# Performance work log

Measured on AMD Instinct MI355X. Metric: run time of the kernel, lower is better.

## Reference

```python
import jax, jax.numpy as jnp
import numpy as np

B, T, N = 32, 512, 16
C, V, D, H, L = 150, 832, 512, 512, 5  # chord vocab, note vocab, embed dim, hidden, layers


def setup_inputs() -> dict:
    key = jax.random.key(0)
    ks = jax.random.split(key, 16)
    s = 0.05
    note = jax.random.randint(ks[0], (B, T, N), 0, V)
    chord = jax.random.randint(ks[1], (B, T), 0, C)
    chord_table = jax.random.normal(ks[2], (C, D), jnp.float32) * s
    note_table = jax.random.normal(ks[3], (V, D), jnp.float32) * s
    # GRU layer 0 (input = 2*D), layers 1..L-1 (input = H), gate order r,z,n like torch
    w_ih0 = jax.random.normal(ks[4], (3 * H, 2 * D), jnp.float32) * s
    w_hh0 = jax.random.normal(ks[5], (3 * H, H), jnp.float32) * s
    b_ih0 = jax.random.normal(ks[6], (3 * H,), jnp.float32) * s
    b_hh0 = jax.random.normal(ks[7], (3 * H,), jnp.float32) * s
    w_ih_r = jax.random.normal(ks[8], (L - 1, 3 * H, H), jnp.float32) * s
    w_hh_r = jax.random.normal(ks[9], (L - 1, 3 * H, H), jnp.float32) * s
    b_ih_r = jax.random.normal(ks[10], (L - 1, 3 * H), jnp.float32) * s
    b_hh_r = jax.random.normal(ks[11], (L - 1, 3 * H), jnp.float32) * s
    fc_w = jax.random.normal(ks[12], (C, H), jnp.float32) * s
    fc_b = jax.random.normal(ks[13], (C,), jnp.float32) * s
    return dict(note=note, chord=chord, chord_table=chord_table, note_table=note_table,
                w_ih0=w_ih0, w_hh0=w_hh0, b_ih0=b_ih0, b_hh0=b_hh0,
                w_ih_r=w_ih_r, w_hh_r=w_hh_r, b_ih_r=b_ih_r, b_hh_r=b_hh_r,
                fc_w=fc_w, fc_b=fc_b)


def _gru_layer(x, wih, whh, bih, bhh):
    # x: [B, T, in] -> [B, T, H], torch GRU cell math (gate order r,z,n)
    xp = jnp.einsum('bti,gi->btg', x, wih) + bih          # precompute input proj [B,T,3H]
    xp = jnp.swapaxes(xp, 0, 1)                            # [T,B,3H]
    h0 = jnp.zeros((x.shape[0], whh.shape[1]), x.dtype)

    def step(h, xpt):
        gh = h @ whh.T + bhh
        xr, xz, xn = jnp.split(xpt, 3, axis=-1)
        hr, hz, hn = jnp.split(gh, 3, axis=-1)
        r = jax.nn.sigmoid(xr + hr)
        z = jax.nn.sigmoid(xz + hz)
        n = jnp.tanh(xn + r * hn)
        h_new = (1.0 - z) * n + z * h
        return h_new, h_new

    _, ys = jax.lax.scan(step, h0, xp)
    return jnp.swapaxes(ys, 0, 1)                          # [B,T,H]


def _forward(note, chord, chord_table, note_table, w_ih0, w_hh0, b_ih0, b_hh0,
             w_ih_r, w_hh_r, b_ih_r, b_hh_r, fc_w, fc_b):
    # padding_idx=0: zero row 0 of both tables (also blocks its gradient)
    ct = chord_table.at[0].set(0.0)
    nt = note_table.at[0].set(0.0)
    chord_emb = ct[chord]                                   # [B,T,D]
    # ragged mean over notes before first zero; mask[k]=1 iff no zero in note[...,:k+1]
    mask = jnp.cumprod((note != 0).astype(chord_table.dtype), axis=-1)  # [B,T,N]
    emb = nt[note]                                          # [B,T,N,D]
    cnt = jnp.maximum(mask.sum(-1), 1.0)                    # zero_index==0 case -> mean of zero row
    note_emb = jnp.einsum('btnd,btn->btd', emb, mask) / cnt[..., None]
    x = jnp.concatenate([chord_emb, note_emb], axis=-1)     # [B,T,2D]
    x = _gru_layer(x, w_ih0, w_hh0, b_ih0, b_hh0)
    for l in range(w_ih_r.shape[0]):
        x = _gru_layer(x, w_ih_r[l], w_hh_r[l], b_ih_r[l], b_hh_r[l])
    return x @ fc_w.T + fc_b                                # [B,T,C]


def reference(note, chord, chord_table, note_table, w_ih0, w_hh0, b_ih0, b_hh0,
              w_ih_r, w_hh_r, b_ih_r, b_hh_r, fc_w, fc_b):
    return _forward(note, chord, chord_table, note_table, w_ih0, w_hh0, b_ih0, b_hh0,
                    w_ih_r, w_hh_r, b_ih_r, b_hh_r, fc_w, fc_b)
```

## Files before the change

kernel.cpp:

```cpp
#include <hip/hip_runtime.h>
#include <hip/hip_bf16.h>

#define B_   32
#define T_   512
#define NN_  16
#define CV_  150
#define D_   512
#define H_   512
#define BT_  16384
#define K0_  1024
#define G3H_ 1536
#define NBF_ 160
#define GXB_ 6144
#define WSZ_ 49152
#define XSLOT_ 16384
#define XRING_ 32
#define HRING_ 8
#define SENT32 0x7f7f7f7fu
#define HCAP 16384
#define XCAP 16384
#define BCAP 65536

using bf16x8 = __attribute__((ext_vector_type(8))) short;
using f32x4  = __attribute__((ext_vector_type(4))) float;
using u32x4  = __attribute__((ext_vector_type(4))) unsigned int;
typedef unsigned long long u64;

__device__ __forceinline__ unsigned short f2bf(float f){
  unsigned int u = __builtin_bit_cast(unsigned int, f);
  u += 0x7fffu + ((u >> 16) & 1u);
  return (unsigned short)(u >> 16);
}

__device__ __forceinline__ void store8(unsigned short* p, f32x4 a, f32x4 b){
  union { unsigned short us[8]; u32x4 v; } u;
  u.us[0]=f2bf(a[0]); u.us[1]=f2bf(a[1]); u.us[2]=f2bf(a[2]); u.us[3]=f2bf(a[3]);
  u.us[4]=f2bf(b[0]); u.us[5]=f2bf(b[1]); u.us[6]=f2bf(b[2]); u.us[7]=f2bf(b[3]);
  *(u32x4*)p = u.v;
}

__device__ __forceinline__ u64 ld_coh_u64(const u64* p){
  return __hip_atomic_load(p, __ATOMIC_RELAXED, __HIP_MEMORY_SCOPE_AGENT);
}
__device__ __forceinline__ void st_coh_u32(void* p, unsigned int v){
  __hip_atomic_store((unsigned int*)p, v, __ATOMIC_RELAXED, __HIP_MEMORY_SCOPE_AGENT);
}
__device__ __forceinline__ float ld_coh_f32(const float* p){
  return __hip_atomic_load(p, __ATOMIC_RELAXED, __HIP_MEMORY_SCOPE_AGENT);
}
__device__ __forceinline__ void st_coh_f32(float* p, float v){
  __hip_atomic_store((unsigned int*)p, __builtin_bit_cast(unsigned int, v),
                     __ATOMIC_RELAXED, __HIP_MEMORY_SCOPE_AGENT);
}
__device__ __forceinline__ void st_flag(int* p, int v){
  __hip_atomic_store(p, v, __ATOMIC_RELAXED, __HIP_MEMORY_SCOPE_AGENT);
}
__device__ __forceinline__ int ld_flag(const int* p){
  return __hip_atomic_load(p, __ATOMIC_RELAXED, __HIP_MEMORY_SCOPE_AGENT);
}

__device__ __forceinline__ bool bad64(u64 q){
  return ((unsigned int)q == SENT32) | ((unsigned int)(q >> 32) == SENT32);
}

__global__ void convert_bf16(const float* __restrict__ src,
                             unsigned short* __restrict__ dst, int n){
  int i = blockIdx.x * 256 + threadIdx.x;
  if (i < n) dst[i] = f2bf(src[i]);
}

__global__ void prep_wfrag(const float* __restrict__ whh0,
                           const float* __restrict__ whhr,
                           const float* __restrict__ wihr,
                           unsigned short* __restrict__ wsw, int total){
  int idx = blockIdx.x * 256 + threadIdx.x;
  if (idx >= total) return;
  int pos = idx & 511;
  int lam = pos >> 3, e = pos & 7;
  int fr  = idx >> 9;
  int ks  = fr & 31;
  int g   = (fr >> 5) % 3;
  int blk = fr / 96;
  int sub = blk & 31, l = blk >> 5;
  int row = g * 512 + sub * 16 + (lam & 15);
  int k   = (ks & 15) * 32 + (lam >> 4) * 8 + e;
  float v;
  if (l == 0) v = (ks < 16) ? whh0[(size_t)row * H_ + k] : 0.f;
  else {
    const float* w = (ks < 16) ? (whhr + (size_t)(l - 1) * G3H_ * H_)
                               : (wihr + (size_t)(l - 1) * G3H_ * H_);
    v = w[(size_t)row * H_ + k];
  }
  wsw[idx] = f2bf(v);
}

__global__ void prep_bias(const float* __restrict__ bhh0,
                          const float* __restrict__ bihr,
                          const float* __restrict__ bhhr,
                          float* __restrict__ bias_sw, int total){
  int idx = blockIdx.x * 256 + threadIdx.x;
  if (idx >= total) return;
  int q = idx & 3, u = (idx >> 2) & 15, sub = (idx >> 6) & 31, l = idx >> 11;
  int j = sub * 16 + u;
  float v;
  if (l == 0){
    v = (q == 0) ? bhh0[j] : (q == 1) ? bhh0[512 + j] : (q == 2) ? 0.f : bhh0[1024 + j];
  } else {
    const float* bi = bihr + (size_t)(l - 1) * G3H_;
    const float* bh = bhhr + (size_t)(l - 1) * G3H_;
    v = (q == 0) ? bi[j] + bh[j]
      : (q == 1) ? bi[512 + j] + bh[512 + j]
      : (q == 2) ? bi[1024 + j] : bh[1024 + j];
  }
  bias_sw[idx] = v;
}

__global__ __launch_bounds__(64) void emb_kernel(
    const int* __restrict__ note, const int* __restrict__ chord,
    const float* __restrict__ ctab, const float* __restrict__ ntab,
    unsigned short* __restrict__ x0){
  const int bt = blockIdx.x;
  const int tid = threadIdx.x;
  __shared__ int sn[NN_];
  if (tid < NN_) sn[tid] = note[bt * NN_ + tid];
  __syncthreads();
  float alive = 1.f, cnt = 0.f;
  float msk[NN_];
  #pragma unroll
  for (int k = 0; k < NN_; ++k){ if (sn[k] == 0) alive = 0.f; msk[k] = alive; cnt += alive; }
  const float inv = 1.f / fmaxf(cnt, 1.f);
  const int ch = chord[bt];
  const int d0 = tid * 8;
  f32x4 c0 = {0.f,0.f,0.f,0.f}, c1 = {0.f,0.f,0.f,0.f};
  if (ch != 0){
    const float* cp = ctab + (size_t)ch * D_ + d0;
    c0 = *(const f32x4*)cp; c1 = *(const f32x4*)(cp + 4);
  }
  f32x4 s0 = {0.f,0.f,0.f,0.f}, s1 = {0.f,0.f,0.f,0.f};
  #pragma unroll
  for (int k = 0; k < NN_; ++k){
    if (msk[k] != 0.f){
      const float* np = ntab + (size_t)sn[k] * D_ + d0;
      s0 += *(const f32x4*)np;
      s1 += *(const f32x4*)(np + 4);
    }
  }
  s0 *= inv; s1 *= inv;
  unsigned short* o = x0 + (size_t)bt * K0_ + d0;
  store8(o, c0, c1);
  store8(o + D_, s0, s1);
}

__global__ __launch_bounds__(256) void gemm_bt(
    const unsigned short* __restrict__ X, const unsigned short* __restrict__ W,
    const float* __restrict__ bias, float* __restrict__ Y,
    int M, int N, int K, int wmode){
  const int lane = threadIdx.x & 63;
  const int wave = threadIdx.x >> 6;
  const int l15 = lane & 15, kq4 = lane >> 4;
  const int m_frag = blockIdx.y * 64 + wave * 16 + l15;
  const int n_base = blockIdx.x * 64;
  f32x4 acc[4] = {{0.f,0.f,0.f,0.f},{0.f,0.f,0.f,0.f},{0.f,0.f,0.f,0.f},{0.f,0.f,0.f,0.f}};
  const unsigned short* xptr = X + (size_t)m_frag * K + kq4 * 8;
  const unsigned short* wptr[4];
  #pragma unroll
  for (int i = 0; i < 4; ++i){
    int n = n_base + i * 16 + l15;
    if (n >= N) n = N - 1;
    wptr[i] = W + (size_t)n * K + kq4 * 8;
  }
  for (int k0 = 0; k0 < K; k0 += 32){
    bf16x8 a = *(const bf16x8*)(xptr + k0);
    #pragma unroll
    for (int i = 0; i < 4; ++i){
      bf16x8 b = *(const bf16x8*)(wptr[i] + k0);
      acc[i] = __builtin_amdgcn_mfma_f32_16x16x32_bf16(a, b, acc[i], 0, 0, 0);
    }
  }
  const int mrow = blockIdx.y * 64 + wave * 16 + kq4 * 4;
  #pragma unroll
  for (int i = 0; i < 4; ++i){
    int n = n_base + i * 16 + l15;
    if (n < N){
      float bv = bias[n];
      #pragma unroll
      for (int r = 0; r < 4; ++r){
        int m = mrow + r;
        float v = acc[i][r] + bv;
        if (wmode == 0) Y[(size_t)m * N + n] = v;
        else            Y[((size_t)(m & (T_-1)) * N + n) * B_ + (m >> 9)] = v;
      }
    }
  }
}

union Ufrag { u64 q[2]; bf16x8 v; };

__global__ __launch_bounds__(256, 1) void gru_fused(
    float* xp, const unsigned short* __restrict__ wsw,
    const float* __restrict__ bias_sw, unsigned short* hT,
    unsigned short* xT, unsigned short* xout, int* cprog,
    const unsigned short* __restrict__ x0g,
    const unsigned short* __restrict__ wih0g,
    const float* __restrict__ bih0g, int* gprog){
  __shared__ unsigned short w_s[96 * 512];
  __shared__ float p_s[2][4][2][2][16][16];

  const int tid = threadIdx.x;
  const int blk = blockIdx.x;

  if (blk >= NBF_){
    const int idx = blk - NBF_;
    const int gx  = idx % 24;
    const int gyy = idx / 24;
    const int bb  = gyy & 31, tc = gyy >> 5;
    const int m0  = bb * 512 + tc * 64;
    const int lane = tid & 63, wave = tid >> 6;
    const int l15 = lane & 15, kq4 = lane >> 4;
    const int m_frag = m0 + wave * 16 + l15;
    const int n_base = gx * 64;
    f32x4 acc[4] = {{0.f,0.f,0.f,0.f},{0.f,0.f,0.f,0.f},{0.f,0.f,0.f,0.f},{0.f,0.f,0.f,0.f}};
    const unsigned short* xptr = x0g + (size_t)m_frag * K0_ + kq4 * 8;
    const unsigned short* wptr[4];
    #pragma unroll
    for (int i = 0; i < 4; ++i){
      int n = n_base + i * 16 + l15;
      wptr[i] = wih0g + (size_t)n * K0_ + kq4 * 8;
    }
    for (int k0 = 0; k0 < K0_; k0 += 32){
      bf16x8 a = *(const bf16x8*)(xptr + k0);
      #pragma unroll
      for (int i = 0; i < 4; ++i){
        bf16x8 b = *(const bf16x8*)(wptr[i] + k0);
        acc[i] = __builtin_amdgcn_mfma_f32_16x16x32_bf16(a, b, acc[i], 0, 0, 0);
      }
    }
    const int mrow = m0 + wave * 16 + kq4 * 4;
    #pragma unroll
    for (int i = 0; i < 4; ++i){
      int n = n_base + i * 16 + l15;
      float bv = bih0g[n];
      #pragma unroll
      for (int r = 0; r < 4; ++r){
        int m = mrow + r;
        float v = acc[i][r] + bv;
        st_coh_f32(&xp[((size_t)(m & (T_-1)) * G3H_ + n) * B_ + (m >> 9)], v);
      }
    }
    asm volatile("s_waitcnt vmcnt(0)" ::: "memory");
    __syncthreads();
    if (tid == 0) atomicAdd(&gprog[tc], 1);
    return;
  }

  const int l   = blk >> 5;
  const int sub = blk & 31;

  {
    const u32x4* src = (const u32x4*)(wsw + (size_t)blk * WSZ_);
    u32x4* dst = (u32x4*)w_s;
    #pragma unroll
    for (int i = 0; i < 24; ++i) dst[tid + 256 * i] = src[tid + 256 * i];
  }
  __syncthreads();

  const int lane = tid & 63, wave = tid >> 6;
  const int l15 = lane & 15, l4 = lane >> 4;
  const int myn = wave >> 1;
  const int kh  = wave & 1;
  const int myb = (myn << 4) + l15;
  const int fro = (l4 << 3);
  const int khofs = kh * 256;
  const int khb = kh * 8;

  const int cb = tid & 31;
  const int cj = (tid >> 5) * 2;
  const int jg = sub * 16 + cj;
  const float* bsp = bias_sw + blk * 64;
  const float br0 = bsp[cj*4+0],     bz0 = bsp[cj*4+1],     bx0 = bsp[cj*4+2],     bn0 = bsp[cj*4+3];
  const float br1 = bsp[(cj+1)*4+0], bz1 = bsp[(cj+1)*4+1], bx1 = bsp[(cj+1)*4+2], bn1 = bsp[(cj+1)*4+3];
  float hres0 = 0.f, hres1 = 0.f;

  unsigned short* hTl = hT + (size_t)l * (HRING_ * 32 * 512);
  unsigned short* xTw = xT + (size_t)(l < 4 ? l : 0) * ((size_t)XRING_ * XSLOT_);
  const unsigned short* xTr = xT + (size_t)(l > 0 ? l - 1 : 0) * ((size_t)XRING_ * XSLOT_);
  const int* bp_own = cprog + (l << 5);
  int*       bp_pub = cprog + ((l > 0 ? l - 1 : 0) << 5);

  float era=0,eza=0,ena=0,era1=0,eza1=0,ena1=0;
  float erb=0,ezb=0,enb=0,erb1=0,ezb1=0,enb1=0;
  if (l == 0){
    if (tid == 0){
      int itc = 0;
      while (ld_flag(&gprog[0]) < 768){
        if (++itc > (1 << 24)) break;
        __builtin_amdgcn_s_sleep(8);
      }
    }
    __syncthreads();
    { const float* xq = xp + (size_t)0 * (G3H_ * B_) + cb;
      era=ld_coh_f32(&xq[(size_t)(0*H_+jg)*B_]); era1=ld_coh_f32(&xq[(size_t)(0*H_+jg+1)*B_]);
      eza=ld_coh_f32(&xq[(size_t)(1*H_+jg)*B_]); eza1=ld_coh_f32(&xq[(size_t)(1*H_+jg+1)*B_]);
      ena=ld_coh_f32(&xq[(size_t)(2*H_+jg)*B_]); ena1=ld_coh_f32(&xq[(size_t)(2*H_+jg+1)*B_]); }
    { const float* xq = xp + (size_t)1 * (G3H_ * B_) + cb;
      erb=ld_coh_f32(&xq[(size_t)(0*H_+jg)*B_]); erb1=ld_coh_f32(&xq[(size_t)(0*H_+jg+1)*B_]);
      ezb=ld_coh_f32(&xq[(size_t)(1*H_+jg)*B_]); ezb1=ld_coh_f32(&xq[(size_t)(1*H_+jg+1)*B_]);
      enb=ld_coh_f32(&xq[(size_t)(2*H_+jg)*B_]); enb1=ld_coh_f32(&xq[(size_t)(2*H_+jg+1)*B_]); }
  }

  for (int t = 0; t < T_; ++t){
    const int pb = t & 1;

    Ufrag xb[8];
    const unsigned short* xs = nullptr;
    if (l > 0){
      xs = xTr + (size_t)(t & (XRING_-1)) * XSLOT_ + (size_t)myb * 512 + khofs + fro;
      #pragma unroll
      for (int j = 0; j < 8; ++j){
        const u64* sp = (const u64*)(xs + (j << 5));
        xb[j].q[0] = ld_coh_u64(sp); xb[j].q[1] = ld_coh_u64(sp + 1);
      }
    }

    Ufrag hb[8];
    const unsigned short* hf = hTl + (((size_t)(t & (HRING_-1)) * 32 + myb) << 9) + khofs + fro;
    #pragma unroll
    for (int j = 0; j < 8; ++j){
      const u64* sp = (const u64*)(hf + (j << 5));
      hb[j].q[0] = ld_coh_u64(sp); hb[j].q[1] = ld_coh_u64(sp + 1);
    }

    if (l < 4 && l > 0 && t && (t & 3) == 0){
      int itc = 0;
      while (true){
        int v = (lane < 32) ? ld_flag(&bp_own[lane]) : 0x7fffffff;
        if (__all(v >= t - 4)) break;
        if (++itc > BCAP) break;
        __builtin_amdgcn_s_sleep(2);
      }
    } else if (l == 0 && t && (t & 3) == 0){
      int itc = 0;
      while (true){
        int v = (lane < 32) ? ld_flag(&bp_own[lane]) : 0x7fffffff;
        if (__all(v >= t - 4)) break;
        if (++itc > BCAP) break;
        __builtin_amdgcn_s_sleep(2);
      }
    }

    f32x4 accR = {0.f,0.f,0.f,0.f}, accZ = {0.f,0.f,0.f,0.f};
    f32x4 accN = {0.f,0.f,0.f,0.f}, accX = {0.f,0.f,0.f,0.f};

    if (l > 0){
      #pragma unroll
      for (int j = 0; j < 8; ++j){
        int itc = 0;
        while (__any((int)(bad64(xb[j].q[0]) | bad64(xb[j].q[1])))){
          if (++itc > XCAP) break;
          if (itc > 2) __builtin_amdgcn_s_sleep(2);
          const u64* sp = (const u64*)(xs + (j << 5));
          xb[j].q[0] = ld_coh_u64(sp); xb[j].q[1] = ld_coh_u64(sp + 1);
        }
        bf16x8 b  = xb[j].v;
        bf16x8 a0 = *(const bf16x8*)&w_s[(0 * 32 + 16 + khb + j) * 512 + lane * 8];
        bf16x8 a1 = *(const bf16x8*)&w_s[(1 * 32 + 16 + khb + j) * 512 + lane * 8];
        bf16x8 a2 = *(const bf16x8*)&w_s[(2 * 32 + 16 + khb + j) * 512 + lane * 8];
        accR = __builtin_amdgcn_mfma_f32_16x16x32_bf16(a0, b, accR, 0, 0, 0);
        accZ = __builtin_amdgcn_mfma_f32_16x16x32_bf16(a1, b, accZ, 0, 0, 0);
        accX = __builtin_amdgcn_mfma_f32_16x16x32_bf16(a2, b, accX, 0, 0, 0);
      }
    }

    #pragma unroll
    for (int j = 0; j < 8; ++j){
      int itc = 0;
      while (__any((int)(bad64(hb[j].q[0]) | bad64(hb[j].q[1])))){
        if (++itc > HCAP) break;
        if (itc > 2) __builtin_amdgcn_s_sleep(2);
        const u64* sp = (const u64*)(hf + (j << 5));
        hb[j].q[0] = ld_coh_u64(sp); hb[j].q[1] = ld_coh_u64(sp + 1);
      }
      bf16x8 b  = hb[j].v;
      bf16x8 a0 = *(const bf16x8*)&w_s[(0 * 32 + khb + j) * 512 + lane * 8];
      bf16x8 a1 = *(const bf16x8*)&w_s[(1 * 32 + khb + j) * 512 + lane * 8];
      bf16x8 a2 = *(const bf16x8*)&w_s[(2 * 32 + khb + j) * 512 + lane * 8];
      accR = __builtin_amdgcn_mfma_f32_16x16x32_bf16(a0, b, accR, 0, 0, 0);
      accZ = __builtin_amdgcn_mfma_f32_16x16x32_bf16(a1, b, accZ, 0, 0, 0);
      accN = __builtin_amdgcn_mfma_f32_16x16x32_bf16(a2, b, accN, 0, 0, 0);
    }

    float erc=0,ezc=0,enc=0,erc1=0,ezc1=0,enc1=0;
    if (l == 0){
      if (((t + 2) & 63) == 0){
        const int ck = ((t + 2) & (T_ - 1)) >> 6;
        if (tid == 0){
          int itc = 0;
          while (ld_flag(&gprog[ck]) < 768){
            if (++itc > (1 << 24)) break;
            __builtin_amdgcn_s_sleep(8);
          }
        }
        __syncthreads();
      }
      const float* xq = xp + (size_t)((t + 2) & (T_ - 1)) * (G3H_ * B_) + cb;
      erc=ld_coh_f32(&xq[(size_t)(0*H_+jg)*B_]); erc1=ld_coh_f32(&xq[(size_t)(0*H_+jg+1)*B_]);
      ezc=ld_coh_f32(&xq[(size_t)(1*H_+jg)*B_]); ezc1=ld_coh_f32(&xq[(size_t)(1*H_+jg+1)*B_]);
      enc=ld_coh_f32(&xq[(size_t)(2*H_+jg)*B_]); enc1=ld_coh_f32(&xq[(size_t)(2*H_+jg+1)*B_]);
    }

    #pragma unroll
    for (int r = 0; r < 4; ++r){
      int u = l4 * 4 + r;
      p_s[pb][0][myn][kh][u][l15] = accR[r];
      p_s[pb][1][myn][kh][u][l15] = accZ[r];
      p_s[pb][2][myn][kh][u][l15] = accN[r];
      p_s[pb][3][myn][kh][u][l15] = accX[r];
    }
    __syncthreads();

    {
      const int nt = cb >> 4, bc = cb & 15;
      float rp0 = p_s[pb][0][nt][0][cj][bc]   + p_s[pb][0][nt][1][cj][bc];
      float rp1 = p_s[pb][0][nt][0][cj+1][bc] + p_s[pb][0][nt][1][cj+1][bc];
      float zp0 = p_s[pb][1][nt][0][cj][bc]   + p_s[pb][1][nt][1][cj][bc];
      float zp1 = p_s[pb][1][nt][0][cj+1][bc] + p_s[pb][1][nt][1][cj+1][bc];
      float hp0 = p_s[pb][2][nt][0][cj][bc]   + p_s[pb][2][nt][1][cj][bc];
      float hp1 = p_s[pb][2][nt][0][cj+1][bc] + p_s[pb][2][nt][1][cj+1][bc];
      float xq0 = p_s[pb][3][nt][0][cj][bc]   + p_s[pb][3][nt][1][cj][bc];
      float xq1 = p_s[pb][3][nt][0][cj+1][bc] + p_s[pb][3][nt][1][cj+1][bc];
      float r0 = 1.f / (1.f + __expf(-(rp0 + era  + br0)));
      float r1 = 1.f / (1.f + __expf(-(rp1 + era1 + br1)));
      float z0 = 1.f / (1.f + __expf(-(zp0 + eza  + bz0)));
      float z1 = 1.f / (1.f + __expf(-(zp1 + eza1 + bz1)));
      float nx0 = (l > 0) ? (xq0 + bx0) : ena;
      float nx1 = (l > 0) ? (xq1 + bx1) : ena1;
      float e0 = __expf(2.f * (nx0 + r0 * (hp0 + bn0)));
      float e1 = __expf(2.f * (nx1 + r1 * (hp1 + bn1)));
      float n0 = (e0 - 1.f) / (e0 + 1.f);
      float n1 = (e1 - 1.f) / (e1 + 1.f);
      float h0 = (1.f - z0) * n0 + z0 * hres0; hres0 = h0;
      float h1 = (1.f - z1) * n1 + z1 * hres1; hres1 = h1;
      unsigned int pk = (unsigned int)f2bf(h0) | ((unsigned int)f2bf(h1) << 16);

      st_coh_u32(hTl + (((size_t)((t + 1) & (HRING_-1)) * 32 + cb) << 9) + jg, pk);
      if (l < 4)
        st_coh_u32(xTw + (size_t)(t & (XRING_-1)) * XSLOT_ + (size_t)cb * 512 + jg, pk);
      else
        *(unsigned int*)&xout[((size_t)cb * T_ + t) * H_ + jg] = pk;
      st_coh_u32(hTl + (((size_t)((t + 4) & (HRING_-1)) * 32 + cb) << 9) + jg, SENT32);
      if (l < 4)
        st_coh_u32(xTw + (size_t)((t + 16) & (XRING_-1)) * XSLOT_ + (size_t)cb * 512 + jg, SENT32);

      if (l > 0 && (t & 3) == 3 && tid == 0) st_flag(&bp_pub[sub], t);

      era = erb; eza = ezb; ena = enb; era1 = erb1; eza1 = ezb1; ena1 = enb1;
      erb = erc; ezb = ezc; enb = enc; erb1 = erc1; ezb1 = ezc1; enb1 = enc1;
    }
  }
}

extern "C" void kernel_launch(void* const* d_in, const int* in_sizes, int n_in,
                              void* d_out, int out_size, void* d_ws, size_t ws_size,
                              hipStream_t stream){
  (void)in_sizes; (void)n_in; (void)out_size; (void)ws_size;
  const int*   note  = (const int*)d_in[0];
  const int*   chord = (const int*)d_in[1];
  const float* ctab  = (const float*)d_in[2];
  const float* ntab  = (const float*)d_in[3];
  const float* wih0  = (const float*)d_in[4];
  const float* whh0  = (const float*)d_in[5];
  const float* bih0  = (const float*)d_in[6];
  const float* bhh0  = (const float*)d_in[7];
  const float* wihr  = (const float*)d_in[8];
  const float* whhr  = (const float*)d_in[9];
  const float* bihr  = (const float*)d_in[10];
  const float* bhhr  = (const float*)d_in[11];
  const float* fcw   = (const float*)d_in[12];
  const float* fcb   = (const float*)d_in[13];
  float* out = (float*)d_out;

  char* ws = (char*)d_ws;
  size_t off = 0;
  auto alloc = [&](size_t bytes)->char*{
    char* p = ws + off; off = (off + bytes + 255) & ~(size_t)255; return p;
  };
  int*            cprog   = (int*)alloc(160 * sizeof(int));
  int*            gprog   = (int*)alloc(8 * sizeof(int));
  float*          xp      = (float*)alloc((size_t)BT_ * G3H_ * 4);
  unsigned short* wsw     = (unsigned short*)alloc((size_t)NBF_ * WSZ_ * 2);
  float*          bias_sw = (float*)alloc((size_t)NBF_ * 64 * 4);
  unsigned short* fcw_b   = (unsigned short*)alloc((size_t)CV_ * H_ * 2);
  unsigned short* xout    = (unsigned short*)alloc((size_t)BT_ * H_ * 2);
  unsigned short* x0      = (unsigned short*)alloc((size_t)BT_ * K0_ * 2);
  unsigned short* wih0_b  = (unsigned short*)alloc((size_t)G3H_ * K0_ * 2);

  const size_t hT_bytes = (size_t)5 * HRING_ * 32 * 512 * 2;
  const size_t hT_al    = (hT_bytes + 255) & ~(size_t)255;
  const size_t xT_bytes = (size_t)4 * XRING_ * XSLOT_ * 2;
  unsigned short* hT = (unsigned short*)d_out;
  unsigned short* xT = (unsigned short*)((char*)d_out + hT_al);

  hipMemsetAsync(cprog, 0, 160 * sizeof(int), stream);
  hipMemsetAsync(gprog, 0, 8 * sizeof(int), stream);
  hipMemsetAsync(hT, 0x7F, hT_bytes, stream);
  for (int ll = 0; ll < 5; ++ll)
    hipMemsetAsync(hT + (size_t)ll * (HRING_ * 32 * 512), 0, 32 * 512 * 2, stream);
  hipMemsetAsync(xT, 0x7F, xT_bytes, stream);

  { int n = G3H_ * K0_; convert_bf16<<<(n + 255) / 256, 256, 0, stream>>>(wih0, wih0_b, n); }
  { int n = CV_ * H_;   convert_bf16<<<(n + 255) / 256, 256, 0, stream>>>(fcw, fcw_b, n); }
  { int n = NBF_ * WSZ_;
    prep_wfrag<<<(n + 255) / 256, 256, 0, stream>>>(whh0, whhr, wihr, wsw, n); }
  { int n = NBF_ * 64;
    prep_bias<<<(n + 255) / 256, 256, 0, stream>>>(bhh0, bihr, bhhr, bias_sw, n); }

  emb_kernel<<<BT_, 64, 0, stream>>>(note, chord, ctab, ntab, x0);

  gru_fused<<<NBF_ + GXB_, 256, 0, stream>>>(xp, wsw, bias_sw, hT, xT, xout, cprog,
                                             x0, wih0_b, bih0, gprog);

  gemm_bt<<<dim3((CV_ + 63) / 64, BT_ / 64), 256, 0, stream>>>(
      xout, fcw_b, fcb, out, BT_, CV_, H_, 0);
}
```

Before: 5.318 ms.

## Fuse FC projection, weight swizzle and bias prep into persistent GRU kernel

Adds FC-output blocks to the persistent GRU launch. They poll a per-subblock progress flag published by layer 4 and compute logits for finished timestep chunks, overlapping the final projection with the tail of the recurrence. Weight fragments and biases are now built directly from the fp32 inputs inside the GRU blocks, which removes the prep_wfrag and prep_bias launches and their intermediate buffers. The hT/xT rings move from the output buffer into workspace so FC blocks can write the output concurrently. This adds spin-wait and coherent-load overhead, and reduces several timeout caps in the wait loops.

```diff
diff --git a/kernel.cpp b/kernel.cpp
--- a/kernel.cpp
+++ b/kernel.cpp
@@ -12,7 +12,7 @@
 #define G3H_ 1536
 #define NBF_ 160
 #define GXB_ 6144
-#define WSZ_ 49152
+#define FCB_ 768
 #define XSLOT_ 16384
 #define XRING_ 32
 #define HRING_ 8
@@ -67,52 +67,6 @@
                              unsigned short* __restrict__ dst, int n){
   int i = blockIdx.x * 256 + threadIdx.x;
   if (i < n) dst[i] = f2bf(src[i]);
-}
-
-__global__ void prep_wfrag(const float* __restrict__ whh0,
-                           const float* __restrict__ whhr,
-                           const float* __restrict__ wihr,
-                           unsigned short* __restrict__ wsw, int total){
-  int idx = blockIdx.x * 256 + threadIdx.x;
-  if (idx >= total) return;
-  int pos = idx & 511;
-  int lam = pos >> 3, e = pos & 7;
-  int fr  = idx >> 9;
-  int ks  = fr & 31;
-  int g   = (fr >> 5) % 3;
-  int blk = fr / 96;
-  int sub = blk & 31, l = blk >> 5;
-  int row = g * 512 + sub * 16 + (lam & 15);
-  int k   = (ks & 15) * 32 + (lam >> 4) * 8 + e;
-  float v;
-  if (l == 0) v = (ks < 16) ? whh0[(size_t)row * H_ + k] : 0.f;
-  else {
-    const float* w = (ks < 16) ? (whhr + (size_t)(l - 1) * G3H_ * H_)
-                               : (wihr + (size_t)(l - 1) * G3H_ * H_);
-    v = w[(size_t)row * H_ + k];
-  }
-  wsw[idx] = f2bf(v);
-}
-
-__global__ void prep_bias(const float* __restrict__ bhh0,
-                          const float* __restrict__ bihr,
-                          const float* __restrict__ bhhr,
-                          float* __restrict__ bias_sw, int total){
-  int idx = blockIdx.x * 256 + threadIdx.x;
-  if (idx >= total) return;
-  int q = idx & 3, u = (idx >> 2) & 15, sub = (idx >> 6) & 31, l = idx >> 11;
-  int j = sub * 16 + u;
-  float v;
-  if (l == 0){
-    v = (q == 0) ? bhh0[j] : (q == 1) ? bhh0[512 + j] : (q == 2) ? 0.f : bhh0[1024 + j];
-  } else {
-    const float* bi = bihr + (size_t)(l - 1) * G3H_;
-    const float* bh = bhhr + (size_t)(l - 1) * G3H_;
-    v = (q == 0) ? bi[j] + bh[j]
-      : (q == 1) ? bi[512 + j] + bh[512 + j]
-      : (q == 2) ? bi[1024 + j] : bh[1024 + j];
-  }
-  bias_sw[idx] = v;
 }
 
 __global__ __launch_bounds__(64) void emb_kernel(
@@ -151,65 +105,25 @@
   store8(o + D_, s0, s1);
 }
 
-__global__ __launch_bounds__(256) void gemm_bt(
-    const unsigned short* __restrict__ X, const unsigned short* __restrict__ W,
-    const float* __restrict__ bias, float* __restrict__ Y,
-    int M, int N, int K, int wmode){
-  const int lane = threadIdx.x & 63;
-  const int wave = threadIdx.x >> 6;
-  const int l15 = lane & 15, kq4 = lane >> 4;
-  const int m_frag = blockIdx.y * 64 + wave * 16 + l15;
-  const int n_base = blockIdx.x * 64;
-  f32x4 acc[4] = {{0.f,0.f,0.f,0.f},{0.f,0.f,0.f,0.f},{0.f,0.f,0.f,0.f},{0.f,0.f,0.f,0.f}};
-  const unsigned short* xptr = X + (size_t)m_frag * K + kq4 * 8;
-  const unsigned short* wptr[4];
-  #pragma unroll
-  for (int i = 0; i < 4; ++i){
-    int n = n_base + i * 16 + l15;
-    if (n >= N) n = N - 1;
-    wptr[i] = W + (size_t)n * K + kq4 * 8;
-  }
-  for (int k0 = 0; k0 < K; k0 += 32){
-    bf16x8 a = *(const bf16x8*)(xptr + k0);
-    #pragma unroll
-    for (int i = 0; i < 4; ++i){
-      bf16x8 b = *(const bf16x8*)(wptr[i] + k0);
-      acc[i] = __builtin_amdgcn_mfma_f32_16x16x32_bf16(a, b, acc[i], 0, 0, 0);
-    }
-  }
-  const int mrow = blockIdx.y * 64 + wave * 16 + kq4 * 4;
-  #pragma unroll
-  for (int i = 0; i < 4; ++i){
-    int n = n_base + i * 16 + l15;
-    if (n < N){
-      float bv = bias[n];
-      #pragma unroll
-      for (int r = 0; r < 4; ++r){
-        int m = mrow + r;
-        float v = acc[i][r] + bv;
-        if (wmode == 0) Y[(size_t)m * N + n] = v;
-        else            Y[((size_t)(m & (T_-1)) * N + n) * B_ + (m >> 9)] = v;
-      }
-    }
-  }
-}
-
 union Ufrag { u64 q[2]; bf16x8 v; };
 
 __global__ __launch_bounds__(256, 1) void gru_fused(
-    float* xp, const unsigned short* __restrict__ wsw,
-    const float* __restrict__ bias_sw, unsigned short* hT,
-    unsigned short* xT, unsigned short* xout, int* cprog,
-    const unsigned short* __restrict__ x0g,
-    const unsigned short* __restrict__ wih0g,
-    const float* __restrict__ bih0g, int* gprog){
+    float* xp, unsigned short* hT, unsigned short* xT, unsigned short* xout,
+    int* cprog, const unsigned short* __restrict__ x0g,
+    const unsigned short* __restrict__ wih0g, const float* __restrict__ bih0g,
+    int* gprog,
+    const float* __restrict__ whh0g, const float* __restrict__ whhrg,
+    const float* __restrict__ wihrg, const float* __restrict__ bhh0g,
+    const float* __restrict__ bihrg, const float* __restrict__ bhhrg,
+    int* l4prog, const unsigned short* __restrict__ fcwbg,
+    const float* __restrict__ fcbg, float* outg){
   __shared__ unsigned short w_s[96 * 512];
   __shared__ float p_s[2][4][2][2][16][16];
 
   const int tid = threadIdx.x;
   const int blk = blockIdx.x;
 
-  if (blk >= NBF_){
+  if (blk >= NBF_ && blk < NBF_ + GXB_){
     const int idx = blk - NBF_;
     const int gx  = idx % 24;
     const int gyy = idx / 24;
@@ -253,14 +167,84 @@
     return;
   }
 
+  if (blk >= NBF_ + GXB_){
+    const int fidx = blk - NBF_ - GXB_;
+    const int fx  = fidx % 3;
+    const int fyy = fidx / 3;
+    const int bb  = fyy & 31, tmc = fyy >> 5;
+    const int m0  = bb * 512 + tmc * 64;
+    const int lane = tid & 63, wave = tid >> 6;
+    const int l15 = lane & 15, kq4 = lane >> 4;
+    const int need = tmc * 64 + 63;
+    {
+      int itc = 0;
+      while (true){
+        int v = (lane < 32) ? ld_flag(&l4prog[lane]) : 0x7fffffff;
+        if (__all(v >= need)) break;
+        if (++itc > (1 << 20)) break;
+        __builtin_amdgcn_s_sleep(8);
+      }
+    }
+    __builtin_amdgcn_sched_barrier(0);
+    const int m_frag = m0 + wave * 16 + l15;
+    f32x4 acc[4] = {{0.f,0.f,0.f,0.f},{0.f,0.f,0.f,0.f},{0.f,0.f,0.f,0.f},{0.f,0.f,0.f,0.f}};
+    const unsigned short* xptr = xout + (size_t)m_frag * H_ + kq4 * 8;
+    const unsigned short* wptr[4];
+    #pragma unroll
+    for (int i = 0; i < 4; ++i){
+      int n = fx * 64 + i * 16 + l15;
+      if (n >= CV_) n = CV_ - 1;
+      wptr[i] = fcwbg + (size_t)n * H_ + kq4 * 8;
+    }
+    for (int k0 = 0; k0 < H_; k0 += 32){
+      Ufrag ua;
+      const u64* sp = (const u64*)(xptr + k0);
+      ua.q[0] = ld_coh_u64(sp); ua.q[1] = ld_coh_u64(sp + 1);
+      bf16x8 a = ua.v;
+      #pragma unroll
+      for (int i = 0; i < 4; ++i){
+        bf16x8 b = *(const bf16x8*)(wptr[i] + k0);
+        acc[i] = __builtin_amdgcn_mfma_f32_16x16x32_bf16(a, b, acc[i], 0, 0, 0);
+      }
+    }
+    const int mrow = m0 + wave * 16 + kq4 * 4;
+    #pragma unroll
+    for (int i = 0; i < 4; ++i){
+      int n = fx * 64 + i * 16 + l15;
+      if (n < CV_){
+        float bv = fcbg[n];
+        #pragma unroll
+        for (int r = 0; r < 4; ++r)
+          outg[(size_t)(mrow + r) * CV_ + n] = acc[i][r] + bv;
+      }
+    }
+    return;
+  }
+
   const int l   = blk >> 5;
   const int sub = blk & 31;
 
   {
-    const u32x4* src = (const u32x4*)(wsw + (size_t)blk * WSZ_);
-    u32x4* dst = (u32x4*)w_s;
-    #pragma unroll
-    for (int i = 0; i < 24; ++i) dst[tid + 256 * i] = src[tid + 256 * i];
+    #pragma unroll 1
+    for (int i = 0; i < 24; ++i){
+      int idx = i * 256 + tid;
+      int fr = idx >> 6, lam = idx & 63;
+      int ks = fr & 31, g = fr >> 5;
+      int row = g * 512 + sub * 16 + (lam & 15);
+      int kcol = (ks & 15) * 32 + ((lam >> 4) << 3);
+      f32x4 a = {0.f,0.f,0.f,0.f}, b2 = {0.f,0.f,0.f,0.f};
+      if (l == 0){
+        if (ks < 16){
+          const float* sp = whh0g + (size_t)row * H_ + kcol;
+          a = *(const f32x4*)sp; b2 = *(const f32x4*)(sp + 4);
+        }
+      } else {
+        const float* wbase = (ks < 16) ? whhrg : wihrg;
+        const float* sp = wbase + (size_t)(l - 1) * G3H_ * H_ + (size_t)row * H_ + kcol;
+        a = *(const f32x4*)sp; b2 = *(const f32x4*)(sp + 4);
+      }
+      store8(&w_s[fr * 512 + lam * 8], a, b2);
+    }
   }
   __syncthreads();
 
@@ -276,9 +260,19 @@
   const int cb = tid & 31;
   const int cj = (tid >> 5) * 2;
   const int jg = sub * 16 + cj;
-  const float* bsp = bias_sw + blk * 64;
-  const float br0 = bsp[cj*4+0],     bz0 = bsp[cj*4+1],     bx0 = bsp[cj*4+2],     bn0 = bsp[cj*4+3];
-  const float br1 = bsp[(cj+1)*4+0], bz1 = bsp[(cj+1)*4+1], bx1 = bsp[(cj+1)*4+2], bn1 = bsp[(cj+1)*4+3];
+
+  float br0, bz0, bx0, bn0, br1, bz1, bx1, bn1;
+  if (l == 0){
+    br0 = bhh0g[jg];       bz0 = bhh0g[512 + jg];     bx0 = 0.f; bn0 = bhh0g[1024 + jg];
+    br1 = bhh0g[jg + 1];   bz1 = bhh0g[512 + jg + 1]; bx1 = 0.f; bn1 = bhh0g[1024 + jg + 1];
+  } else {
+    const float* bi = bihrg + (size_t)(l - 1) * G3H_;
+    const float* bh = bhhrg + (size_t)(l - 1) * G3H_;
+    br0 = bi[jg] + bh[jg];           bz0 = bi[512 + jg] + bh[512 + jg];
+    bx0 = bi[1024 + jg];             bn0 = bh[1024 + jg];
+    br1 = bi[jg + 1] + bh[jg + 1];   bz1 = bi[512 + jg + 1] + bh[512 + jg + 1];
+    bx1 = bi[1024 + jg + 1];         bn1 = bh[1024 + jg + 1];
+  }
   float hres0 = 0.f, hres1 = 0.f;
 
   unsigned short* hTl = hT + (size_t)l * (HRING_ * 32 * 512);
@@ -293,7 +287,7 @@
     if (tid == 0){
       int itc = 0;
       while (ld_flag(&gprog[0]) < 768){
-        if (++itc > (1 << 24)) break;
+        if (++itc > (1 << 20)) break;
         __builtin_amdgcn_s_sleep(8);
       }
     }
@@ -330,15 +324,7 @@
       hb[j].q[0] = ld_coh_u64(sp); hb[j].q[1] = ld_coh_u64(sp + 1);
     }
 
-    if (l < 4 && l > 0 && t && (t & 3) == 0){
-      int itc = 0;
-      while (true){
-        int v = (lane < 32) ? ld_flag(&bp_own[lane]) : 0x7fffffff;
-        if (__all(v >= t - 4)) break;
-        if (++itc > BCAP) break;
-        __builtin_amdgcn_s_sleep(2);
-      }
-    } else if (l == 0 && t && (t & 3) == 0){
+    if (l < 4 && t && (t & 3) == 0){
       int itc = 0;
       while (true){
         int v = (lane < 32) ? ld_flag(&bp_own[lane]) : 0x7fffffff;
@@ -396,7 +382,7 @@
         if (tid == 0){
           int itc = 0;
           while (ld_flag(&gprog[ck]) < 768){
-            if (++itc > (1 << 24)) break;
+            if (++itc > (1 << 20)) break;
             __builtin_amdgcn_s_sleep(8);
           }
         }
@@ -446,17 +432,20 @@
       if (l < 4)
         st_coh_u32(xTw + (size_t)(t & (XRING_-1)) * XSLOT_ + (size_t)cb * 512 + jg, pk);
       else
-        *(unsigned int*)&xout[((size_t)cb * T_ + t) * H_ + jg] = pk;
+        st_coh_u32(&xout[((size_t)cb * T_ + t) * H_ + jg], pk);
       st_coh_u32(hTl + (((size_t)((t + 4) & (HRING_-1)) * 32 + cb) << 9) + jg, SENT32);
       if (l < 4)
         st_coh_u32(xTw + (size_t)((t + 16) & (XRING_-1)) * XSLOT_ + (size_t)cb * 512 + jg, SENT32);
 
       if (l > 0 && (t & 3) == 3 && tid == 0) st_flag(&bp_pub[sub], t);
+      if (l == 4 && (t & 3) == 3 && tid == 0) st_flag(&l4prog[sub], t - 1);
 
       era = erb; eza = ezb; ena = enb; era1 = erb1; eza1 = ezb1; ena1 = enb1;
       erb = erc; ezb = ezc; enb = enc; erb1 = erc1; ezb1 = ezc1; enb1 = enc1;
     }
   }
+  __syncthreads();
+  if (l == 4 && tid == 0) st_flag(&l4prog[sub], T_ - 1);
 }
 
 extern "C" void kernel_launch(void* const* d_in, const int* in_sizes, int n_in,
@@ -486,22 +475,20 @@
   };
   int*            cprog   = (int*)alloc(160 * sizeof(int));
   int*            gprog   = (int*)alloc(8 * sizeof(int));
+  int*            l4prog  = (int*)alloc(32 * sizeof(int));
   float*          xp      = (float*)alloc((size_t)BT_ * G3H_ * 4);
-  unsigned short* wsw     = (unsigned short*)alloc((size_t)NBF_ * WSZ_ * 2);
-  float*          bias_sw = (float*)alloc((size_t)NBF_ * 64 * 4);
   unsigned short* fcw_b   = (unsigned short*)alloc((size_t)CV_ * H_ * 2);
   unsigned short* xout    = (unsigned short*)alloc((size_t)BT_ * H_ * 2);
   unsigned short* x0      = (unsigned short*)alloc((size_t)BT_ * K0_ * 2);
   unsigned short* wih0_b  = (unsigned short*)alloc((size_t)G3H_ * K0_ * 2);
-
   const size_t hT_bytes = (size_t)5 * HRING_ * 32 * 512 * 2;
-  const size_t hT_al    = (hT_bytes + 255) & ~(size_t)255;
   const size_t xT_bytes = (size_t)4 * XRING_ * XSLOT_ * 2;
-  unsigned short* hT = (unsigned short*)d_out;
-  unsigned short* xT = (unsigned short*)((char*)d_out + hT_al);
+  unsigned short* hT      = (unsigned short*)alloc(hT_bytes);
+  unsigned short* xT      = (unsigned short*)alloc(xT_bytes);
 
   hipMemsetAsync(cprog, 0, 160 * sizeof(int), stream);
   hipMemsetAsync(gprog, 0, 8 * sizeof(int), stream);
+  hipMemsetAsync(l4prog, 0xFF, 32 * sizeof(int), stream);
   hipMemsetAsync(hT, 0x7F, hT_bytes, stream);
   for (int ll = 0; ll < 5; ++ll)
     hipMemsetAsync(hT + (size_t)ll * (HRING_ * 32 * 512), 0, 32 * 512 * 2, stream);
@@ -509,16 +496,10 @@
 
   { int n = G3H_ * K0_; convert_bf16<<<(n + 255) / 256, 256, 0, stream>>>(wih0, wih0_b, n); }
   { int n = CV_ * H_;   convert_bf16<<<(n + 255) / 256, 256, 0, stream>>>(fcw, fcw_b, n); }
-  { int n = NBF_ * WSZ_;
-    prep_wfrag<<<(n + 255) / 256, 256, 0, stream>>>(whh0, whhr, wihr, wsw, n); }
-  { int n = NBF_ * 64;
-    prep_bias<<<(n + 255) / 256, 256, 0, stream>>>(bhh0, bihr, bhhr, bias_sw, n); }
 
   emb_kernel<<<BT_, 64, 0, stream>>>(note, chord, ctab, ntab, x0);
 
-  gru_fused<<<NBF_ + GXB_, 256, 0, stream>>>(xp, wsw, bias_sw, hT, xT, xout, cprog,
-                                             x0, wih0_b, bih0, gprog);
-
-  gemm_bt<<<dim3((CV_ + 63) / 64, BT_ / 64), 256, 0, stream>>>(
-      xout, fcw_b, fcb, out, BT_, CV_, H_, 0);
-}
+  gru_fused<<<NBF_ + GXB_ + FCB_, 256, 0, stream>>>(
+      xp, hT, xT, xout, cprog, x0, wih0_b, bih0, gprog,
+      whh0, whhr, wihr, bhh0, bihr, bhhr, l4prog, fcw_b, fcb, out);
+}
```

Result: no change. 5.414 ms (+1.8%).
